# Kernel tuning notes

Hardware: AMD Instinct MI355X
Metric: run time of the kernel (lower is better)

The kernel has to match this reference:

```python
import jax, jax.numpy as jnp
import numpy as np

B, N0, FEAT, NHID, GDIM = 32, 2048, 1036, 128, 32
DEG = 16
E = B * N0 * DEG
K1, K2, K3 = 410, 82, 17  # ceil(0.2*{2048,410,82}) per SAGPooling stage


def _segsum(v, idx, n):
    return jax.ops.segment_sum(v, idx, num_segments=n)


def sage_conv(x, src, dst, em, Wl, bl, Wr, n):
    # PyG SAGEConv: lin_l(mean_{j->i} x_j) + lin_r(x_i); lin applied before the
    # (linear) mean -> identical math, messages are NHID-dim not FEAT-dim.
    h = x @ Wl
    s = _segsum(h[src] * em[:, None], dst, n)
    cnt = _segsum(em, dst, n)
    return s / jnp.maximum(cnt, 1.0)[:, None] + bl + x @ Wr


def gcn_score(x, src, dst, em, W, b, n):
    # 1-channel GCNConv with self-loops and symmetric normalization.
    h = x @ W  # [n, 1]
    deg = 1.0 + _segsum(em, dst, n)  # +1 for self loop
    dis = jax.lax.rsqrt(deg)
    norm = dis[src] * dis[dst] * em
    agg = _segsum(h[src] * norm[:, None], dst, n) + h / deg[:, None]
    return (agg + b)[:, 0]


def sag_pool(x, src, dst, em, W, b, n_per, k):
    # Equal-size graphs -> static top-k per graph; dropped edges masked, not removed.
    nb = x.shape[0] // n_per
    score = gcn_score(x, src, dst, em, W, b, x.shape[0])
    _, idx = jax.lax.top_k(score.reshape(nb, n_per), k)
    perm = (idx + (jnp.arange(nb) * n_per)[:, None]).reshape(-1)
    xn = x[perm] * jnp.tanh(score[perm])[:, None]
    inv = jnp.full((x.shape[0],), -1, jnp.int32).at[perm].set(
        jnp.arange(nb * k, dtype=jnp.int32))
    ns, nd = inv[src], inv[dst]
    emn = em * ((ns >= 0) & (nd >= 0)).astype(em.dtype)
    return xn, jnp.maximum(ns, 0), jnp.maximum(nd, 0), emn


def readout(x, k):
    r = x.reshape(B, k, NHID)
    return jnp.concatenate([r.max(axis=1), r.mean(axis=1)], axis=1)  # [B, 2*NHID]


def graphnet(x, src, dst, W1l, b1l, W1r, Wp1, bp1, W2l, b2l, W2r, Wp2, bp2,
             W3l, b3l, W3r, Wp3, bp3, lin1_w, lin1_b, lin2_w, lin2_b, lin3_w, lin3_b):
    # NormalizeFeaturesV2: first 12 cols / column max
    mx = jnp.max(x[:, :12], axis=0)
    x = jnp.concatenate([x[:, :12] / mx, x[:, 12:]], axis=1)
    em = jnp.ones((E,), x.dtype)

    x = jax.nn.relu(sage_conv(x, src, dst, em, W1l, b1l, W1r, B * N0))
    x, s1, d1, e1 = sag_pool(x, src, dst, em, Wp1, bp1, N0, K1)
    x1 = readout(x, K1)

    x = jax.nn.relu(sage_conv(x, s1, d1, e1, W2l, b2l, W2r, B * K1))
    x, s2, d2, e2 = sag_pool(x, s1, d1, e1, Wp2, bp2, K1, K2)
    x2 = readout(x, K2)

    x = jax.nn.relu(sage_conv(x, s2, d2, e2, W3l, b3l, W3r, B * K2))
    x, s3, d3, e3 = sag_pool(x, s2, d2, e2, Wp3, bp3, K2, K3)
    x3 = readout(x, K3)

    h = x1 + x2 + x3
    h = jax.nn.relu(h @ lin1_w + lin1_b)  # dropout is identity at eval
    features = jax.nn.relu(h @ lin2_w + lin2_b)
    out = features @ lin3_w + lin3_b  # act=None
    return features, out


def setup_inputs():
    key = jax.random.key(0)
    ks = jax.random.split(key, 16)
    x = jax.random.normal(ks[0], (B * N0, FEAT), jnp.float32)
    e = jax.random.randint(ks[1], (2, B, N0 * DEG), 0, N0)
    ei = (e + (jnp.arange(B) * N0)[None, :, None]).reshape(2, -1).astype(jnp.int32)

    def lin(k, fi, fo):
        return (jax.random.normal(k, (fi, fo), jnp.float32) / np.sqrt(fi)).astype(jnp.float32)

    z = lambda *s: jnp.zeros(s, jnp.float32)
    return dict(
        x=x, src=ei[0], dst=ei[1],
        W1l=lin(ks[2], FEAT, NHID), b1l=z(NHID), W1r=lin(ks[3], FEAT, NHID),
        Wp1=lin(ks[4], NHID, 1), bp1=z(1),
        W2l=lin(ks[5], NHID, NHID), b2l=z(NHID), W2r=lin(ks[6], NHID, NHID),
        Wp2=lin(ks[7], NHID, 1), bp2=z(1),
        W3l=lin(ks[8], NHID, NHID), b3l=z(NHID), W3r=lin(ks[9], NHID, NHID),
        Wp3=lin(ks[10], NHID, 1), bp3=z(1),
        lin1_w=lin(ks[11], 2 * NHID, NHID), lin1_b=z(NHID),
        lin2_w=lin(ks[12], NHID, GDIM), lin2_b=z(GDIM),
        lin3_w=lin(ks[13], GDIM, 1), lin3_b=z(1),
    )


def reference(x, src, dst, W1l, b1l, W1r, Wp1, bp1, W2l, b2l, W2r, Wp2, bp2,
              W3l, b3l, W3r, Wp3, bp3, lin1_w, lin1_b, lin2_w, lin2_b, lin3_w, lin3_b):
    return graphnet(x, src, dst, W1l, b1l, W1r, Wp1, bp1, W2l, b2l, W2r, Wp2, bp2,
                    W3l, b3l, W3r, Wp3, bp3, lin1_w, lin1_b, lin2_w, lin2_b,
                    lin3_w, lin3_b)
```

## Files before the change

kernel.cpp:

```cpp
#include <hip/hip_runtime.h>

typedef unsigned int u32;
typedef unsigned short u16;

#define NB 32
#define N0V 2048
#define FEATV 1036
#define EDGESV (NB*N0V*16)
#define KK1 410
#define KK2 82
#define KK3 17
#define NN1 (NB*N0V)
#define NN2 (NB*KK1)
#define NN3 (NB*KK2)
#define NN4 (NB*KK3)
#define KSTEP1 33
#define KSTEP2 4
#define ESTR 32768

typedef __bf16 bf16x8 __attribute__((ext_vector_type(8)));
typedef float f32x4 __attribute__((ext_vector_type(4)));

__device__ inline u16 f2bf(float f){
  u32 u = __float_as_uint(f);
  u32 r = (u + 0x7FFFu + ((u >> 16) & 1u)) >> 16;
  return (u16)r;
}
__device__ inline float bf2f(u16 h){ return __uint_as_float(((u32)h) << 16); }
__device__ inline float dec_ord(u32 u){
  u32 bits = (u & 0x80000000u) ? (u ^ 0x80000000u) : ~u;
  return __uint_as_float(bits);
}
__device__ inline void gload_lds16(const void* g, void* l){
  __builtin_amdgcn_global_load_lds(
      (const __attribute__((address_space(1))) unsigned int*)g,
      (__attribute__((address_space(3))) unsigned int*)l, 16, 0, 0);
}
__device__ inline void cvt4(float4 v, ushort4& h, ushort4& l){
  h.x=f2bf(v.x); l.x=f2bf(v.x-bf2f(h.x));
  h.y=f2bf(v.y); l.y=f2bf(v.y-bf2f(h.y));
  h.z=f2bf(v.z); l.z=f2bf(v.z-bf2f(h.z));
  h.w=f2bf(v.w); l.w=f2bf(v.w-bf2f(h.w));
}

__global__ void init_kernel(u32* mx){
  if (threadIdx.x < 12) mx[threadIdx.x] = 0;
}

__global__ void colmax_kernel(const float* __restrict__ x, u32* mx){
  __shared__ float sm[256];
  int t = threadIdx.x;
  int r = blockIdx.x*256 + t;
  const float4* p = (const float4*)(x + (size_t)r*FEATV);
  float4 v0 = p[0], v1 = p[1], v2 = p[2];
  float m[12] = {v0.x,v0.y,v0.z,v0.w, v1.x,v1.y,v1.z,v1.w, v2.x,v2.y,v2.z,v2.w};
  for (int j=0;j<12;j++){
    sm[t] = m[j]; __syncthreads();
    for (int off=128; off>0; off>>=1){ if (t<off) sm[t]=fmaxf(sm[t],sm[t+off]); __syncthreads(); }
    if (t==0){
      u32 b = __float_as_uint(sm[0]);
      u32 u = (b & 0x80000000u) ? ~b : (b | 0x80000000u);
      atomicMax(&mx[j], u);
    }
    __syncthreads();
  }
}

__global__ void wprep_all(const float* __restrict__ W1l, const float* __restrict__ W1r,
                          const float* __restrict__ W2l, const float* __restrict__ W2r,
                          const float* __restrict__ W3l, const float* __restrict__ W3r,
                          const u32* __restrict__ mxo,
                          u16* __restrict__ B1h, u16* __restrict__ B1l,
                          u16* __restrict__ B2h, u16* __restrict__ B2l,
                          u16* __restrict__ B3h, u16* __restrict__ B3l){
  int idx = blockIdx.x*256 + threadIdx.x;
  const float *Wl, *Wr; u16 *oh, *ol; int K, o, scale12;
  if (idx < KSTEP1*8192){ Wl=W1l; Wr=W1r; oh=B1h; ol=B1l; K=FEATV; o=idx; scale12=1; }
  else if (idx < (KSTEP1+KSTEP2)*8192){ Wl=W2l; Wr=W2r; oh=B2h; ol=B2l; K=128; o=idx-KSTEP1*8192; scale12=0; }
  else if (idx < (KSTEP1+2*KSTEP2)*8192){ Wl=W3l; Wr=W3r; oh=B3h; ol=B3l; K=128; o=idx-(KSTEP1+KSTEP2)*8192; scale12=0; }
  else return;
  int kt = o >> 13, r13 = o & 8191;
  int khg = r13 >> 11, n = (r13 >> 3) & 255, kk8 = r13 & 7;
  int k = (kt << 5) + khg*8 + kk8;
  float v = 0.f;
  if (k < K) v = (n < 128) ? Wl[(size_t)k*128 + n] : Wr[(size_t)k*128 + (n-128)];
  if (scale12 && k < 12) v /= dec_ord(mxo[k]);
  u16 h = f2bf(v);
  oh[o] = h;
  ol[o] = f2bf(v - bf2f(h));
}

__launch_bounds__(256, 2)
__global__ void gemm_csr_kernel(const float* __restrict__ A, int lda, int M,
                                int Kvalid, int Ksteps,
                                const u16* __restrict__ Bth, const u16* __restrict__ Btl,
                                float* __restrict__ C,
                                const int* __restrict__ srcE, const int* __restrict__ dstE,
                                const int* ecnt_in, int globalIds, int nperCsr,
                                int* __restrict__ rps, int* __restrict__ rpd,
                                int* __restrict__ adjW){
  __shared__ __align__(16) u16 Ah[2][2048];
  __shared__ __align__(16) u16 Al[2][2048];
  __shared__ __align__(16) u16 Bh[2][8192];
  __shared__ __align__(16) u16 Bl[2][8192];
  int tid = threadIdx.x;

  if ((int)blockIdx.x < NB){
    int g = blockIdx.x;
    int* cnt  = (int*)&Bh[0][0];
    int* part = (int*)&Bl[0][0];
    int ne = ecnt_in ? ecnt_in[g] : ESTR;
    size_t eb = (size_t)g*ESTR;
    for (int i = tid; i < nperCsr; i += 256) cnt[i] = 0;
    __syncthreads();
    int goff = globalIds ? g*nperCsr : 0;
    int addB = globalIds ? 0 : g*nperCsr;
    for (int e = tid; e < ne; e += 256) atomicAdd(&cnt[dstE[eb+e] - goff], 1);
    __syncthreads();
    int chunk = (nperCsr + 255) >> 8;
    int c0 = tid*chunk, ssum = 0;
    for (int u = 0; u < chunk; ++u){ int i = c0+u; if (i < nperCsr) ssum += cnt[i]; }
    part[tid] = ssum;
    __syncthreads();
    for (int off = 1; off < 256; off <<= 1){
      int v = (tid >= off) ? part[tid-off] : 0;
      __syncthreads();
      part[tid] += v;
      __syncthreads();
    }
    int run = part[tid] - ssum;
    for (int u = 0; u < chunk; ++u){
      int i = c0+u;
      if (i < nperCsr){
        int c = cnt[i];
        rps[g*nperCsr + i] = (int)(g*ESTR + run);
        rpd[g*nperCsr + i] = c;
        cnt[i] = run;
        run += c;
      }
    }
    __syncthreads();
    for (int e = tid; e < ne; e += 256){
      int d = dstE[eb+e], s = srcE[eb+e];
      int p = atomicAdd(&cnt[d - goff], 1);
      adjW[eb + p] = s + addB;
    }
    return;
  }

  int row0 = ((int)blockIdx.x - NB) * 64;
  int w = tid >> 6, lane = tid & 63;
  int lr = lane & 15, kh = lane >> 4;

  int p0i = tid, p1i = tid + 256;
  int kg0 = p0i >> 7, rw0 = (p0i & 127) >> 1, hf0 = p0i & 1;
  int kg1 = p1i >> 7, rw1 = (p1i & 127) >> 1, hf1 = p1i & 1;
  int coff0 = kg0*8 + hf0*4, coff1 = kg1*8 + hf1*4;
  const float* pA0 = A + (size_t)(row0 + rw0)*lda + coff0;
  const float* pA1 = A + (size_t)(row0 + rw1)*lda + coff1;
  int wi0 = kg0*512 + rw0*8 + hf0*4;
  int wi1 = kg1*512 + rw1*8 + hf1*4;

  f32x4 acc[4][4];
  #pragma unroll
  for (int i=0;i<4;i++)
    #pragma unroll
    for (int j=0;j<4;j++) acc[i][j] = (f32x4){0.f,0.f,0.f,0.f};

  float4 z4 = make_float4(0.f,0.f,0.f,0.f);

#define LOADA(KT, V0, V1) { int k0_ = (KT)<<5; \
    V0 = (k0_ + coff0 < Kvalid) ? *(const float4*)(pA0 + k0_) : z4; \
    V1 = (k0_ + coff1 < Kvalid) ? *(const float4*)(pA1 + k0_) : z4; }

#define ISSUEB(KT, BUF) { size_t tb_ = (size_t)(KT)*8192; \
    _Pragma("unroll") \
    for (int j_=0;j_<4;j_++){ int o_ = j_*2048 + w*512; \
      gload_lds16(Bth + tb_ + o_ + lane*8, &Bh[BUF][o_]); \
      gload_lds16(Btl + tb_ + o_ + lane*8, &Bl[BUF][o_]); } }

#define CVTWRITE(V0, V1, BUF) { ushort4 h_, l_; \
    cvt4(V0, h_, l_); *(ushort4*)&Ah[BUF][wi0] = h_; *(ushort4*)&Al[BUF][wi0] = l_; \
    cvt4(V1, h_, l_); *(ushort4*)&Ah[BUF][wi1] = h_; *(ushort4*)&Al[BUF][wi1] = l_; }

  float4 a0, a1, pp0, pp1;
  LOADA(0, a0, a1);
  ISSUEB(0, 0);
  LOADA(1, pp0, pp1);
  CVTWRITE(a0, a1, 0);
  asm volatile("s_waitcnt lgkmcnt(0)" ::: "memory");
  asm volatile("s_waitcnt vmcnt(2)" ::: "memory");
  __builtin_amdgcn_s_barrier();

  for (int kt = 0; kt < Ksteps; ++kt){
    int cur = kt & 1, nxt = cur ^ 1;
    if (kt+1 < Ksteps) ISSUEB(kt+1, nxt);
    float4 n0 = z4, n1 = z4;
    if (kt+2 < Ksteps) LOADA(kt+2, n0, n1);
    if (kt+2 < Ksteps)      asm volatile("s_waitcnt vmcnt(12)" ::: "memory");
    else if (kt+1 < Ksteps) asm volatile("s_waitcnt vmcnt(10)" ::: "memory");
    else                    asm volatile("s_waitcnt vmcnt(0)"  ::: "memory");
    __builtin_amdgcn_sched_barrier(0);

    bf16x8 fah[4], fal[4], fbh[4], fbl[4];
    #pragma unroll
    for (int ni=0;ni<4;ni++){
      int idx = kh*2048 + (w*64 + ni*16 + lr)*8;
      fbh[ni] = *(const bf16x8*)&Bh[cur][idx];
      fbl[ni] = *(const bf16x8*)&Bl[cur][idx];
    }
    #pragma unroll
    for (int mi=0;mi<2;mi++){
      int idx = kh*512 + (mi*16 + lr)*8;
      fah[mi] = *(const bf16x8*)&Ah[cur][idx];
      fal[mi] = *(const bf16x8*)&Al[cur][idx];
    }
    __builtin_amdgcn_sched_barrier(0);
    if (kt+1 < Ksteps) CVTWRITE(pp0, pp1, nxt);
    __builtin_amdgcn_sched_barrier(0);
    #pragma unroll
    for (int mi=2;mi<4;mi++){
      int idx = kh*512 + (mi*16 + lr)*8;
      fah[mi] = *(const bf16x8*)&Ah[cur][idx];
      fal[mi] = *(const bf16x8*)&Al[cur][idx];
    }
    asm volatile("s_waitcnt lgkmcnt(8)" ::: "memory");
    __builtin_amdgcn_sched_barrier(0);
    __builtin_amdgcn_s_setprio(1);
    #pragma unroll
    for (int mi=0;mi<2;mi++)
      #pragma unroll
      for (int ni=0;ni<4;ni++){
        acc[mi][ni] = __builtin_amdgcn_mfma_f32_16x16x32_bf16(fah[mi], fbh[ni], acc[mi][ni], 0,0,0);
        acc[mi][ni] = __builtin_amdgcn_mfma_f32_16x16x32_bf16(fah[mi], fbl[ni], acc[mi][ni], 0,0,0);
        acc[mi][ni] = __builtin_amdgcn_mfma_f32_16x16x32_bf16(fal[mi], fbh[ni], acc[mi][ni], 0,0,0);
      }
    __builtin_amdgcn_s_setprio(0);
    asm volatile("s_waitcnt lgkmcnt(0)" ::: "memory");
    __builtin_amdgcn_sched_barrier(0);
    __builtin_amdgcn_s_setprio(1);
    #pragma unroll
    for (int mi=2;mi<4;mi++)
      #pragma unroll
      for (int ni=0;ni<4;ni++){
        acc[mi][ni] = __builtin_amdgcn_mfma_f32_16x16x32_bf16(fah[mi], fbh[ni], acc[mi][ni], 0,0,0);
        acc[mi][ni] = __builtin_amdgcn_mfma_f32_16x16x32_bf16(fah[mi], fbl[ni], acc[mi][ni], 0,0,0);
        acc[mi][ni] = __builtin_amdgcn_mfma_f32_16x16x32_bf16(fal[mi], fbh[ni], acc[mi][ni], 0,0,0);
      }
    __builtin_amdgcn_s_setprio(0);
    pp0 = n0; pp1 = n1;
    __builtin_amdgcn_s_barrier();
  }
#undef LOADA
#undef ISSUEB
#undef CVTWRITE
  #pragma unroll
  for (int mi=0;mi<4;mi++)
    #pragma unroll
    for (int j=0;j<4;j++){
      int row = row0 + mi*16 + kh*4 + j;
      #pragma unroll
      for (int ni=0;ni<4;ni++){
        int col = w*64 + ni*16 + lr;
        C[(size_t)row*256 + col] = acc[mi][ni][j];
      }
    }
}

__global__ void convfin_w(const float* __restrict__ hcomb, const int* __restrict__ rps,
                          const int* __restrict__ rpd, const int* __restrict__ adj,
                          const float* __restrict__ bl, const float* __restrict__ Wp,
                          float* __restrict__ xout, float* __restrict__ hsc,
                          int nper, int bpg, int xcdMap){
  int b = blockIdx.x, t = threadIdx.x;
  int g, slot;
  if (xcdMap){ int xcd = b & 7, idx = b >> 3; g = xcd + 8*(idx >> 8); slot = idx & 255; }
  else { g = b / bpg; slot = b - g*bpg; }
  int wv = t >> 6, lane = t & 63;
  int sub = lane >> 5, l32 = lane & 31;
  int i = slot*8 + wv*2 + sub;
  if (i >= nper) return;
  int gi = g*nper + i;
  int s = rps[gi], d = rpd[gi];
  float4 a = make_float4(0.f,0.f,0.f,0.f);
  for (int e = s; e < s+d; ++e){
    float4 hj = *(const float4*)(hcomb + (size_t)adj[e]*256 + l32*4);
    a.x += hj.x; a.y += hj.y; a.z += hj.z; a.w += hj.w;
  }
  float invc = 1.0f / fmaxf((float)d, 1.0f);
  float4 hr = *(const float4*)(hcomb + (size_t)gi*256 + 128 + l32*4);
  float4 bb = *(const float4*)(bl + l32*4);
  float4 o;
  o.x = fmaxf(a.x*invc + bb.x + hr.x, 0.f);
  o.y = fmaxf(a.y*invc + bb.y + hr.y, 0.f);
  o.z = fmaxf(a.z*invc + bb.z + hr.z, 0.f);
  o.w = fmaxf(a.w*invc + bb.w + hr.w, 0.f);
  *(float4*)(xout + (size_t)gi*128 + l32*4) = o;
  float4 wp = *(const float4*)(Wp + l32*4);
  float v = o.x*wp.x + o.y*wp.y + o.z*wp.z + o.w*wp.w;
  #pragma unroll
  for (int m = 16; m > 0; m >>= 1) v += __shfl_xor(v, m);
  if (l32 == 0) hsc[gi] = v;
}

__global__ void scoreagg_w(const float* __restrict__ hsc, const int* __restrict__ rps,
                           const int* __restrict__ rpd, const int* __restrict__ adj,
                           const float* __restrict__ bp, int nper, int ntot,
                           u32* __restrict__ su){
  int gi = blockIdx.x*256 + threadIdx.x;
  if (gi >= ntot) return;
  float di = 1.0f + (float)rpd[gi];
  float a = hsc[gi] / di;
  float rdi = rsqrtf(di);
  int s = rps[gi], d = rpd[gi];
  for (int e = s; e < s+d; ++e){
    int j = adj[e];
    a += hsc[j] * rsqrtf(1.0f + (float)rpd[j]) * rdi;
  }
  float sc = a + bp[0];
  u32 b = __float_as_uint(sc);
  su[gi] = (b & 0x80000000u) ? ~b : (b | 0x80000000u);
}

__launch_bounds__(512)
__global__ void topkpool(const u32* __restrict__ suG, const float* __restrict__ xin,
                         int nper, int k,
                         float* __restrict__ xp, float* __restrict__ r,
                         int* __restrict__ invG, int* __restrict__ ecnt_next){
  __shared__ u32 su[2048];
  __shared__ int bins[256], sfx[256];
  __shared__ int slist[416];
  __shared__ int tlist[64];
  __shared__ float smx[512], ssm[512];
  __shared__ u32 spfx;
  __shared__ int srem, ssel, stie;
  int g = blockIdx.x, t = threadIdx.x;
  int gbase = g*nper;
  for (int i = t; i < nper; i += 512){
    su[i] = suG[gbase + i];
    invG[gbase + i] = -1;
  }
  if (t == 0){ spfx = 0; srem = k; ssel = 0; stie = 0; if (ecnt_next) ecnt_next[g] = 0; }
  __syncthreads();
  for (int pass = 0; pass < 4; ++pass){
    int shift = 24 - 8*pass;
    if (t < 256) bins[t] = 0;
    __syncthreads();
    u32 pfx = spfx; int rem = srem;
    for (int i = t; i < nper; i += 512){
      u32 u = su[i];
      if (pass == 0 || (u >> (shift+8)) == (pfx >> (shift+8)))
        atomicAdd(&bins[(u >> shift) & 255], 1);
    }
    __syncthreads();
    if (t < 256) sfx[t] = bins[t];
    __syncthreads();
    for (int off=1; off<256; off<<=1){
      int v = 0;
      if (t < 256 && t + off < 256) v = sfx[t+off];
      __syncthreads();
      if (t < 256) sfx[t] += v;
      __syncthreads();
    }
    if (t < 256){
      int above = (t == 255) ? 0 : sfx[t+1];
      if (sfx[t] >= rem && above < rem){
        spfx = pfx | ((u32)t << shift);
        srem = rem - above;
      }
    }
    __syncthreads();
  }
  u32 th = spfx;
  for (int i = t; i < nper; i += 512)
    if (su[i] > th){ int p = atomicAdd(&ssel, 1); slist[p] = i; }
  __syncthreads();
  for (int i = t; i < nper; i += 512)
    if (su[i] == th){ int q = atomicAdd(&stie, 1); if (q < 64) tlist[q] = i; }
  __syncthreads();
  if (t == 0){
    int p = ssel, need = k - p;
    if (need > 0){
      if (stie <= 64){
        for (int a = 1; a < stie; ++a){
          int v = tlist[a], b2 = a-1;
          while (b2 >= 0 && tlist[b2] > v){ tlist[b2+1] = tlist[b2]; b2--; }
          tlist[b2+1] = v;
        }
        for (int m = 0; m < need; ++m) slist[p+m] = tlist[m];
      } else {
        for (int i = 0; i < nper && p < k; ++i)
          if (su[i] == th) slist[p++] = i;
      }
    }
  }
  __syncthreads();
  int q = t >> 7, c = t & 127;
  float mxv = -3.4e38f, smv = 0.f;
  for (int j = q; j < k; j += 4){
    int li = slist[j];
    float ts = tanhf(dec_ord(su[li]));
    float vv = xin[((size_t)(gbase + li))*128 + c] * ts;
    xp[((size_t)(g*k + j))*128 + c] = vv;
    mxv = fmaxf(mxv, vv); smv += vv;
  }
  smx[t] = mxv; ssm[t] = smv;
  for (int j = t; j < k; j += 512) invG[gbase + slist[j]] = j;
  __syncthreads();
  if (t < 128){
    r[g*256 + t] = fmaxf(fmaxf(smx[t], smx[t+128]), fmaxf(smx[t+256], smx[t+384]));
    r[g*256 + 128 + t] = (ssm[t]+ssm[t+128]+ssm[t+256]+ssm[t+384]) / (float)k;
  }
}

__global__ void compactw(const int* __restrict__ srcE, const int* __restrict__ dstE,
                         const int* ecnt_in, int inGlobal, int nperIn,
                         const int* __restrict__ invG,
                         int* __restrict__ osrc, int* __restrict__ odst,
                         int* __restrict__ cursor){
  int b = blockIdx.x;
  int g = b >> 4, sl = b & 15;
  int ne = ecnt_in ? ecnt_in[g] : ESTR;
  int e0 = sl*2048;
  if (e0 >= ne) return;
  int e1 = min(e0 + 2048, ne);
  size_t eb = (size_t)g*ESTR;
  int gadd = inGlobal ? 0 : g*nperIn;
  for (int e = e0 + threadIdx.x; e < e1; e += 256){
    int s = srcE[eb+e] + gadd, d = dstE[eb+e] + gadd;
    int ns = invG[s], nd = invG[d];
    if (ns >= 0 && nd >= 0){
      int p = atomicAdd(&cursor[g], 1);
      osrc[eb + p] = ns; odst[eb + p] = nd;
    }
  }
}

__global__ void head_kernel(const float* __restrict__ r1, const float* __restrict__ r2,
                            const float* __restrict__ r3,
                            const float* __restrict__ w1, const float* __restrict__ b1,
                            const float* __restrict__ w2, const float* __restrict__ b2,
                            const float* __restrict__ w3, const float* __restrict__ b3,
                            float* __restrict__ out){
  __shared__ float hs[32][256];
  __shared__ float h1[32][128];
  __shared__ float ft[32][32];
  int t = threadIdx.x;
  for (int o = t; o < 32*256; o += 256) hs[o>>8][o&255] = r1[o]+r2[o]+r3[o];
  __syncthreads();
  for (int o = t; o < 32*128; o += 256){
    int i = o >> 7, j = o & 127;
    float a = b1[j];
    for (int c = 0; c < 256; ++c) a += hs[i][c]*w1[c*128 + j];
    h1[i][j] = fmaxf(a, 0.f);
  }
  __syncthreads();
  for (int o = t; o < 32*32; o += 256){
    int i = o >> 5, j = o & 31;
    float a = b2[j];
    for (int c = 0; c < 128; ++c) a += h1[i][c]*w2[c*32 + j];
    float v = fmaxf(a, 0.f);
    ft[i][j] = v;
    out[o] = v;
  }
  __syncthreads();
  if (t < 32){
    float a = b3[0];
    for (int c = 0; c < 32; ++c) a += ft[t][c]*w3[c];
    out[1024 + t] = a;
  }
}

extern "C" void kernel_launch(void* const* d_in, const int* in_sizes, int n_in,
                              void* d_out, int out_size, void* d_ws, size_t ws_size,
                              hipStream_t stream){
  (void)in_sizes; (void)n_in; (void)out_size; (void)ws_size;
  const float* x   = (const float*)d_in[0];
  const int* esrc  = (const int*)d_in[1];
  const int* edst  = (const int*)d_in[2];
  const float* W1l = (const float*)d_in[3];
  const float* b1l = (const float*)d_in[4];
  const float* W1r = (const float*)d_in[5];
  const float* Wp1 = (const float*)d_in[6];
  const float* bp1 = (const float*)d_in[7];
  const float* W2l = (const float*)d_in[8];
  const float* b2l = (const float*)d_in[9];
  const float* W2r = (const float*)d_in[10];
  const float* Wp2 = (const float*)d_in[11];
  const float* bp2 = (const float*)d_in[12];
  const float* W3l = (const float*)d_in[13];
  const float* b3l = (const float*)d_in[14];
  const float* W3r = (const float*)d_in[15];
  const float* Wp3 = (const float*)d_in[16];
  const float* bp3 = (const float*)d_in[17];
  const float* l1w = (const float*)d_in[18];
  const float* l1b = (const float*)d_in[19];
  const float* l2w = (const float*)d_in[20];
  const float* l2b = (const float*)d_in[21];
  const float* l3w = (const float*)d_in[22];
  const float* l3b = (const float*)d_in[23];
  float* out = (float*)d_out;

  char* ws = (char*)d_ws;
  size_t off = 0;
  auto alloc = [&](size_t bytes)->char*{
    char* p = ws + off; off = (off + bytes + 255) & ~(size_t)255; return p;
  };

  u32* mx     = (u32*)alloc(64);
  int* ecnt1g = (int*)alloc(NB*4);
  int* ecnt2g = (int*)alloc(NB*4);
  int* rps   = (int*)alloc((size_t)NN1*4);
  int* rpd   = (int*)alloc((size_t)NN1*4);
  int* adj   = (int*)alloc((size_t)EDGESV*4);
  int* eAs   = (int*)alloc((size_t)EDGESV*4);
  int* eAd   = (int*)alloc((size_t)EDGESV*4);
  int* eBs   = (int*)alloc((size_t)EDGESV*4);
  int* eBd   = (int*)alloc((size_t)EDGESV*4);
  u16* B1h   = (u16*)alloc((size_t)KSTEP1*8192*2);
  u16* B1l   = (u16*)alloc((size_t)KSTEP1*8192*2);
  u16* B2h   = (u16*)alloc((size_t)KSTEP2*8192*2);
  u16* B2l   = (u16*)alloc((size_t)KSTEP2*8192*2);
  u16* B3h   = (u16*)alloc((size_t)KSTEP2*8192*2);
  u16* B3l   = (u16*)alloc((size_t)KSTEP2*8192*2);
  float* hcomb = (float*)alloc((size_t)NN1*256*4);
  float* x1    = (float*)alloc((size_t)NN1*128*4);
  float* x2    = (float*)alloc((size_t)NN2*128*4);
  float* x3    = (float*)alloc((size_t)NN3*128*4);
  float* xp1   = (float*)alloc((size_t)NN2*128*4);
  float* xp2   = (float*)alloc((size_t)NN3*128*4);
  float* xp3   = (float*)alloc((size_t)NN4*128*4);
  float* hsc   = (float*)alloc((size_t)NN1*4);
  u32* suG     = (u32*)alloc((size_t)NN1*4);
  int* invG    = (int*)alloc((size_t)NN1*4);
  float* r1    = (float*)alloc((size_t)32*256*4);
  float* r2    = (float*)alloc((size_t)32*256*4);
  float* r3    = (float*)alloc((size_t)32*256*4);

  init_kernel<<<1, 64, 0, stream>>>(mx);
  colmax_kernel<<<256, 256, 0, stream>>>(x, mx);
  wprep_all<<<((KSTEP1+2*KSTEP2)*8192+255)/256, 256, 0, stream>>>(
      W1l, W1r, W2l, W2r, W3l, W3r, mx, B1h, B1l, B2h, B2l, B3h, B3l);

  gemm_csr_kernel<<<NB + NN1/64, 256, 0, stream>>>(
      x, FEATV, NN1, FEATV, KSTEP1, B1h, B1l, hcomb,
      esrc, edst, nullptr, 1, N0V, rps, rpd, adj);
  convfin_w<<<NN1/8, 256, 0, stream>>>(hcomb, rps, rpd, adj, b1l, Wp1, x1, hsc, N0V, 256, 1);
  scoreagg_w<<<NN1/256, 256, 0, stream>>>(hsc, rps, rpd, adj, bp1, N0V, NN1, suG);
  topkpool<<<NB, 512, 0, stream>>>(suG, x1, N0V, KK1, xp1, r1, invG, ecnt1g);
  compactw<<<NB*16, 256, 0, stream>>>(esrc, edst, nullptr, 1, N0V, invG, eAs, eAd, ecnt1g);

  gemm_csr_kernel<<<NB + (NN2+63)/64, 256, 0, stream>>>(
      xp1, 128, NN2, 128, KSTEP2, B2h, B2l, hcomb,
      eAs, eAd, ecnt1g, 0, KK1, rps, rpd, adj);
  convfin_w<<<NB*52, 256, 0, stream>>>(hcomb, rps, rpd, adj, b2l, Wp2, x2, hsc, KK1, 52, 0);
  scoreagg_w<<<(NN2+255)/256, 256, 0, stream>>>(hsc, rps, rpd, adj, bp2, KK1, NN2, suG);
  topkpool<<<NB, 512, 0, stream>>>(suG, x2, KK1, KK2, xp2, r2, invG, ecnt2g);
  compactw<<<NB*16, 256, 0, stream>>>(eAs, eAd, ecnt1g, 0, KK1, invG, eBs, eBd, ecnt2g);

  gemm_csr_kernel<<<NB + (NN3+63)/64, 256, 0, stream>>>(
      xp2, 128, NN3, 128, KSTEP2, B3h, B3l, hcomb,
      eBs, eBd, ecnt2g, 0, KK2, rps, rpd, adj);
  convfin_w<<<NB*11, 256, 0, stream>>>(hcomb, rps, rpd, adj, b3l, Wp3, x3, hsc, KK2, 11, 0);
  scoreagg_w<<<(NN3+255)/256, 256, 0, stream>>>(hsc, rps, rpd, adj, bp3, KK2, NN3, suG);
  topkpool<<<NB, 512, 0, stream>>>(suG, x3, KK2, KK3, xp3, r3, invG, nullptr);

  head_kernel<<<1, 256, 0, stream>>>(r1, r2, r3, l1w, l1b, l2w, l2b, l3w, l3b, out);
}
```

Measured before the change: 570.9 us.

## Load GEMM B fragments directly from global into registers, dropping LDS staging

The B operand (pre-split bf16 hi/lo weights) is no longer staged through double-buffered LDS with global_load_lds. Each wave now reads its B fragments straight from global memory (L2-resident) into registers every k-step. The freed LDS lets launch bounds rise to 3 blocks per CU, and the A conversion uses the native bf16 casts. The MFMA phase is also simplified into a single block. Latency of the B loads is no longer hidden behind the previous step, so each k-step may stall on global reads even with higher occupancy.

```diff
diff --git a/kernel.cpp b/kernel.cpp
--- a/kernel.cpp
+++ b/kernel.cpp
@@ -31,16 +31,13 @@
   u32 bits = (u & 0x80000000u) ? (u ^ 0x80000000u) : ~u;
   return __uint_as_float(bits);
 }
-__device__ inline void gload_lds16(const void* g, void* l){
-  __builtin_amdgcn_global_load_lds(
-      (const __attribute__((address_space(1))) unsigned int*)g,
-      (__attribute__((address_space(3))) unsigned int*)l, 16, 0, 0);
-}
-__device__ inline void cvt4(float4 v, ushort4& h, ushort4& l){
-  h.x=f2bf(v.x); l.x=f2bf(v.x-bf2f(h.x));
-  h.y=f2bf(v.y); l.y=f2bf(v.y-bf2f(h.y));
-  h.z=f2bf(v.z); l.z=f2bf(v.z-bf2f(h.z));
-  h.w=f2bf(v.w); l.w=f2bf(v.w-bf2f(h.w));
+__device__ inline u16 bfbits(__bf16 b){ union{__bf16 f; u16 u;} c; c.f=b; return c.u; }
+__device__ inline void cvt4c(float4 v, ushort4& h, ushort4& l){
+  __bf16 h0=(__bf16)v.x, h1=(__bf16)v.y, h2=(__bf16)v.z, h3=(__bf16)v.w;
+  float r0=v.x-(float)h0, r1=v.y-(float)h1, r2=v.z-(float)h2, r3=v.w-(float)h3;
+  h.x=bfbits(h0); h.y=bfbits(h1); h.z=bfbits(h2); h.w=bfbits(h3);
+  l.x=bfbits((__bf16)r0); l.y=bfbits((__bf16)r1);
+  l.z=bfbits((__bf16)r2); l.w=bfbits((__bf16)r3);
 }
 
 __global__ void init_kernel(u32* mx){
@@ -90,7 +87,7 @@
   ol[o] = f2bf(v - bf2f(h));
 }
 
-__launch_bounds__(256, 2)
+__launch_bounds__(256, 3)
 __global__ void gemm_csr_kernel(const float* __restrict__ A, int lda, int M,
                                 int Kvalid, int Ksteps,
                                 const u16* __restrict__ Bth, const u16* __restrict__ Btl,
@@ -101,14 +98,12 @@
                                 int* __restrict__ adjW){
   __shared__ __align__(16) u16 Ah[2][2048];
   __shared__ __align__(16) u16 Al[2][2048];
-  __shared__ __align__(16) u16 Bh[2][8192];
-  __shared__ __align__(16) u16 Bl[2][8192];
   int tid = threadIdx.x;
 
   if ((int)blockIdx.x < NB){
     int g = blockIdx.x;
-    int* cnt  = (int*)&Bh[0][0];
-    int* part = (int*)&Bl[0][0];
+    int* cnt  = (int*)&Ah[0][0];
+    int* part = (int*)&Al[0][0];
     int ne = ecnt_in ? ecnt_in[g] : ESTR;
     size_t eb = (size_t)g*ESTR;
     for (int i = tid; i < nperCsr; i += 256) cnt[i] = 0;
@@ -161,6 +156,9 @@
   int wi0 = kg0*512 + rw0*8 + hf0*4;
   int wi1 = kg1*512 + rw1*8 + hf1*4;
 
+  const u16* bph = Bth + kh*2048 + (w*64 + lr)*8;
+  const u16* bpl = Btl + kh*2048 + (w*64 + lr)*8;
+
   f32x4 acc[4][4];
   #pragma unroll
   for (int i=0;i<4;i++)
@@ -173,74 +171,42 @@
     V0 = (k0_ + coff0 < Kvalid) ? *(const float4*)(pA0 + k0_) : z4; \
     V1 = (k0_ + coff1 < Kvalid) ? *(const float4*)(pA1 + k0_) : z4; }
 
-#define ISSUEB(KT, BUF) { size_t tb_ = (size_t)(KT)*8192; \
-    _Pragma("unroll") \
-    for (int j_=0;j_<4;j_++){ int o_ = j_*2048 + w*512; \
-      gload_lds16(Bth + tb_ + o_ + lane*8, &Bh[BUF][o_]); \
-      gload_lds16(Btl + tb_ + o_ + lane*8, &Bl[BUF][o_]); } }
-
 #define CVTWRITE(V0, V1, BUF) { ushort4 h_, l_; \
-    cvt4(V0, h_, l_); *(ushort4*)&Ah[BUF][wi0] = h_; *(ushort4*)&Al[BUF][wi0] = l_; \
-    cvt4(V1, h_, l_); *(ushort4*)&Ah[BUF][wi1] = h_; *(ushort4*)&Al[BUF][wi1] = l_; }
+    cvt4c(V0, h_, l_); *(ushort4*)&Ah[BUF][wi0] = h_; *(ushort4*)&Al[BUF][wi0] = l_; \
+    cvt4c(V1, h_, l_); *(ushort4*)&Ah[BUF][wi1] = h_; *(ushort4*)&Al[BUF][wi1] = l_; }
 
   float4 a0, a1, pp0, pp1;
   LOADA(0, a0, a1);
-  ISSUEB(0, 0);
   LOADA(1, pp0, pp1);
   CVTWRITE(a0, a1, 0);
   asm volatile("s_waitcnt lgkmcnt(0)" ::: "memory");
-  asm volatile("s_waitcnt vmcnt(2)" ::: "memory");
   __builtin_amdgcn_s_barrier();
 
   for (int kt = 0; kt < Ksteps; ++kt){
     int cur = kt & 1, nxt = cur ^ 1;
-    if (kt+1 < Ksteps) ISSUEB(kt+1, nxt);
+    const u16* bh_p = bph + (size_t)kt*8192;
+    const u16* bl_p = bpl + (size_t)kt*8192;
+    bf16x8 fbh[4], fbl[4];
+    #pragma unroll
+    for (int ni=0;ni<4;ni++){
+      fbh[ni] = *(const bf16x8*)(bh_p + ni*128);
+      fbl[ni] = *(const bf16x8*)(bl_p + ni*128);
+    }
     float4 n0 = z4, n1 = z4;
     if (kt+2 < Ksteps) LOADA(kt+2, n0, n1);
-    if (kt+2 < Ksteps)      asm volatile("s_waitcnt vmcnt(12)" ::: "memory");
-    else if (kt+1 < Ksteps) asm volatile("s_waitcnt vmcnt(10)" ::: "memory");
-    else                    asm volatile("s_waitcnt vmcnt(0)"  ::: "memory");
-    __builtin_amdgcn_sched_barrier(0);
-
-    bf16x8 fah[4], fal[4], fbh[4], fbl[4];
+    bf16x8 fah[4], fal[4];
     #pragma unroll
-    for (int ni=0;ni<4;ni++){
-      int idx = kh*2048 + (w*64 + ni*16 + lr)*8;
-      fbh[ni] = *(const bf16x8*)&Bh[cur][idx];
-      fbl[ni] = *(const bf16x8*)&Bl[cur][idx];
-    }
-    #pragma unroll
-    for (int mi=0;mi<2;mi++){
+    for (int mi=0;mi<4;mi++){
       int idx = kh*512 + (mi*16 + lr)*8;
       fah[mi] = *(const bf16x8*)&Ah[cur][idx];
       fal[mi] = *(const bf16x8*)&Al[cur][idx];
     }
-    __builtin_amdgcn_sched_barrier(0);
     if (kt+1 < Ksteps) CVTWRITE(pp0, pp1, nxt);
-    __builtin_amdgcn_sched_barrier(0);
-    #pragma unroll
-    for (int mi=2;mi<4;mi++){
-      int idx = kh*512 + (mi*16 + lr)*8;
-      fah[mi] = *(const bf16x8*)&Ah[cur][idx];
-      fal[mi] = *(const bf16x8*)&Al[cur][idx];
-    }
-    asm volatile("s_waitcnt lgkmcnt(8)" ::: "memory");
-    __builtin_amdgcn_sched_barrier(0);
-    __builtin_amdgcn_s_setprio(1);
-    #pragma unroll
-    for (int mi=0;mi<2;mi++)
-      #pragma unroll
-      for (int ni=0;ni<4;ni++){
-        acc[mi][ni] = __builtin_amdgcn_mfma_f32_16x16x32_bf16(fah[mi], fbh[ni], acc[mi][ni], 0,0,0);
-        acc[mi][ni] = __builtin_amdgcn_mfma_f32_16x16x32_bf16(fah[mi], fbl[ni], acc[mi][ni], 0,0,0);
-        acc[mi][ni] = __builtin_amdgcn_mfma_f32_16x16x32_bf16(fal[mi], fbh[ni], acc[mi][ni], 0,0,0);
-      }
-    __builtin_amdgcn_s_setprio(0);
     asm volatile("s_waitcnt lgkmcnt(0)" ::: "memory");
     __builtin_amdgcn_sched_barrier(0);
     __builtin_amdgcn_s_setprio(1);
     #pragma unroll
-    for (int mi=2;mi<4;mi++)
+    for (int mi=0;mi<4;mi++)
       #pragma unroll
       for (int ni=0;ni<4;ni++){
         acc[mi][ni] = __builtin_amdgcn_mfma_f32_16x16x32_bf16(fah[mi], fbh[ni], acc[mi][ni], 0,0,0);
@@ -252,7 +218,6 @@
     __builtin_amdgcn_s_barrier();
   }
 #undef LOADA
-#undef ISSUEB
 #undef CVTWRITE
   #pragma unroll
   for (int mi=0;mi<4;mi++)
```

After: 588.2 us. 3.0% more time.
